# Performance work log

Measured on AMD Instinct MI355X. Metric: run time of the kernel, lower is better.

## Reference

```python
import jax, jax.numpy as jnp
import numpy as np

EPS = 1e-8


def setup_inputs() -> dict:
    key = jax.random.key(0)
    k1, k2, k3 = jax.random.split(key, 3)
    Nq, Nr = 16384, 16384
    return {
        "query_points": jax.random.normal(k1, (Nq, 3), dtype=jnp.float32),
        "ref_points": jax.random.normal(k2, (Nr, 3), dtype=jnp.float32),
        "ref_flow": jax.random.normal(k3, (Nr, 3), dtype=jnp.float32),
        "k": 3,
    }


def reference(query_points, ref_points, ref_flow, k):
    # torch.cdist: Euclidean distance matrix [Nq, Nr]
    q2 = jnp.sum(query_points * query_points, axis=-1, keepdims=True)   # [Nq,1]
    r2 = jnp.sum(ref_points * ref_points, axis=-1)                      # [Nr]
    d2 = q2 + r2[None, :] - 2.0 * (query_points @ ref_points.T)        # [Nq,Nr]
    dist = jnp.sqrt(jnp.maximum(d2, 0.0))
    # topk smallest distances
    neg_top, knn_idx = jax.lax.top_k(-dist, k)                          # [Nq,k]
    knn_dist = -neg_top
    # inverse-distance weights, normalized
    weights = 1.0 / (knn_dist + EPS)
    weights = weights / jnp.sum(weights, axis=1, keepdims=True)
    # gather neighbor flows and reduce: [Nq,k,3] -> [Nq,3]
    knn_flow = ref_flow[knn_idx]
    return jnp.sum(weights[..., None] * knn_flow, axis=1)
```

## Files before the change

kernel.cpp:

```cpp
#include <hip/hip_runtime.h>
#include <math.h>

#define G      32
#define NCELLS (G * G * G)
#define LOF    (-6.0f)
#define HH     0.375f
#define INVH   (1.0f / 0.375f)
#define DELTA  1e-3f
#define NCHUNK 16
#define R2ACC  (HH * HH)
#define SCB    128
#define SCC    (NCELLS / SCB)

__device__ __forceinline__ int cell_coord(float x) {
    int c = (int)floorf((x - LOF) * INVH);
    c = c < 0 ? 0 : c;
    return c > G - 1 ? G - 1 : c;
}
__device__ __forceinline__ int imax2(int a, int b) { return a > b ? a : b; }
__device__ __forceinline__ int imin2(int a, int b) { return a < b ? a : b; }
__device__ __forceinline__ float rdfl(float v) {
    return __int_as_float(__builtin_amdgcn_readfirstlane(__float_as_int(v)));
}

#define LEXINSERT(dv, jv) do {                                        \
    float d_ = (dv); int j_ = (jv);                                   \
    bool l0 = (d_ < e0) || ((d_ == e0) && (j_ < i0));                 \
    bool l1 = (d_ < e1) || ((d_ == e1) && (j_ < i1));                 \
    bool l2 = (d_ < e2) || ((d_ == e2) && (j_ < i2));                 \
    int   ni0 = l0 ? j_ : i0;                                         \
    int   ni1 = l0 ? i0 : (l1 ? j_ : i1);                             \
    int   ni2 = l1 ? i1 : (l2 ? j_ : i2);                             \
    float ne0 = l0 ? d_ : e0;                                         \
    float ne1 = l0 ? e0 : (l1 ? d_ : e1);                             \
    float ne2 = l1 ? e1 : (l2 ? d_ : e2);                             \
    e0 = ne0; e1 = ne1; e2 = ne2; i0 = ni0; i1 = ni1; i2 = ni2;       \
} while (0)

#define SCAN_RUN(lo_, hi_) do {                                       \
    for (int u = (lo_) + lane; u < (hi_); u += 64) {                  \
        float4 rr = srt[u];                                           \
        float xx = rr.x * rr.x;                                       \
        float yy = rr.y * rr.y;                                       \
        float zz = rr.z * rr.z;                                       \
        float r2 = (xx + yy) + zz;                                    \
        float td = qx * rr.x;                                         \
        td = fmaf(qy, rr.y, td);                                      \
        td = fmaf(qz, rr.z, td);                                      \
        float aa = q2 + r2;                                           \
        float dd = fmaf(-2.0f, td, aa);                               \
        int jj = __float_as_int(rr.w);                                \
        LEXINSERT(dd, jj);                                            \
    }                                                                 \
} while (0)

#define MERGE64() do {                                                \
    _Pragma("unroll")                                                 \
    for (int mk_ = 1; mk_ < 64; mk_ <<= 1) {                          \
        float f0 = __shfl_xor(e0, mk_, 64);                           \
        float f1 = __shfl_xor(e1, mk_, 64);                           \
        float f2 = __shfl_xor(e2, mk_, 64);                           \
        int   g0 = __shfl_xor(i0, mk_, 64);                           \
        int   g1 = __shfl_xor(i1, mk_, 64);                           \
        int   g2 = __shfl_xor(i2, mk_, 64);                           \
        LEXINSERT(f0, g0);                                            \
        LEXINSERT(f1, g1);                                            \
        LEXINSERT(f2, g2);                                            \
    }                                                                 \
} while (0)

#define MERGE32() do {                                                \
    _Pragma("unroll")                                                 \
    for (int mk_ = 1; mk_ < 32; mk_ <<= 1) {                          \
        float f0 = __shfl_xor(e0, mk_, 64);                           \
        float f1 = __shfl_xor(e1, mk_, 64);                           \
        float f2 = __shfl_xor(e2, mk_, 64);                           \
        int   g0 = __shfl_xor(i0, mk_, 64);                           \
        int   g1 = __shfl_xor(i1, mk_, 64);                           \
        int   g2 = __shfl_xor(i2, mk_, 64);                           \
        LEXINSERT(f0, g0);                                            \
        LEXINSERT(f1, g1);                                            \
        LEXINSERT(f2, g2);                                            \
    }                                                                 \
} while (0)

#define EPILOGUE() do {                                               \
    e0 = fmaxf(e0, 0.0f);                                             \
    e1 = fmaxf(e1, 0.0f);                                             \
    e2 = fmaxf(e2, 0.0f);                                             \
    float s0 = sqrtf(e0);                                             \
    float s1 = sqrtf(e1);                                             \
    float s2 = sqrtf(e2);                                             \
    float w0 = 1.0f / (s0 + 1e-8f);                                   \
    float w1 = 1.0f / (s1 + 1e-8f);                                   \
    float w2 = 1.0f / (s2 + 1e-8f);                                   \
    float wsum = (w0 + w1) + w2;                                      \
    w0 = w0 / wsum; w1 = w1 / wsum; w2 = w2 / wsum;                   \
    float f0x = flow[i0*3+0], f0y = flow[i0*3+1], f0z = flow[i0*3+2]; \
    float f1x = flow[i1*3+0], f1y = flow[i1*3+1], f1z = flow[i1*3+2]; \
    float f2x = flow[i2*3+0], f2y = flow[i2*3+1], f2z = flow[i2*3+2]; \
    out[q*3+0] = (w0 * f0x + w1 * f1x) + w2 * f2x;                    \
    out[q*3+1] = (w0 * f0y + w1 * f1y) + w2 * f2y;                    \
    out[q*3+2] = (w0 * f0z + w1 * f1z) + w2 * f2z;                    \
} while (0)

__global__ __launch_bounds__(256) void zero_ints(int* __restrict__ p, int n) {
    int i = blockIdx.x * 256 + threadIdx.x;
    if (i < n) p[i] = 0;
}

__global__ __launch_bounds__(256) void bin_count(
    const float* __restrict__ ref, int* __restrict__ cnt, int Nr) {
    int j = blockIdx.x * 256 + threadIdx.x;
    if (j >= Nr) return;
    int cx = cell_coord(ref[3 * j + 0]);
    int cy = cell_coord(ref[3 * j + 1]);
    int cz = cell_coord(ref[3 * j + 2]);
    atomicAdd(&cnt[(cz * G + cy) * G + cx], 1);
}

__global__ __launch_bounds__(256) void scan1(
    const int* __restrict__ cnt, int* __restrict__ off, int* __restrict__ bsum) {
    __shared__ int wt[4];
    int tid = threadIdx.x, b = blockIdx.x;
    int base = b * SCC;
    int lane = tid & 63, wid = tid >> 6;
    int v = cnt[base + tid];
    int incl = v;
#pragma unroll
    for (int sh = 1; sh < 64; sh <<= 1) {
        int t = __shfl_up(incl, sh, 64);
        if (lane >= sh) incl += t;
    }
    if (lane == 63) wt[wid] = incl;
    __syncthreads();
    if (tid == 0) {
        int run = 0;
#pragma unroll
        for (int w = 0; w < 4; ++w) { int t = wt[w]; wt[w] = run; run += t; }
    }
    __syncthreads();
    int excl = wt[wid] + incl - v;
    off[base + tid] = excl;
    if (tid == SCC - 1) bsum[b] = excl + v;
}

__global__ __launch_bounds__(256) void scan2(
    const int* __restrict__ bsum, int* __restrict__ off, int* __restrict__ cur) {
    __shared__ int red[4];
    __shared__ int bo;
    int tid = threadIdx.x, b = blockIdx.x;
    int lane = tid & 63, wid = tid >> 6;
    int m = (tid < b) ? bsum[tid] : 0;
#pragma unroll
    for (int mk = 1; mk < 64; mk <<= 1) m += __shfl_xor(m, mk, 64);
    if (lane == 0) red[wid] = m;
    __syncthreads();
    if (tid == 0) bo = red[0] + red[1] + red[2] + red[3];
    __syncthreads();
    int boff = bo;
    int base = b * SCC;
    int t = off[base + tid] + boff;
    off[base + tid] = t;
    cur[base + tid] = t;
    if (b == SCB - 1 && tid == SCC - 1) off[NCELLS] = boff + bsum[b];
}

__global__ __launch_bounds__(256) void bin_fill(
    const float* __restrict__ ref, int* __restrict__ cur,
    float4* __restrict__ srt, int Nr) {
    int j = blockIdx.x * 256 + threadIdx.x;
    if (j >= Nr) return;
    float x = ref[3 * j + 0], y = ref[3 * j + 1], z = ref[3 * j + 2];
    int cx = cell_coord(x), cy = cell_coord(y), cz = cell_coord(z);
    int cell = (cz * G + cy) * G + cx;
    int pos = atomicAdd(&cur[cell], 1);
    srt[pos] = make_float4(x, y, z, __int_as_float(j));
}

#define MAPIDX(u_, out_) do {                                         \
    int t_ = (u_) + b0;                                               \
    t_ = ((u_) >= p1) ? ((u_) + b1) : t_;                             \
    t_ = ((u_) >= p2) ? ((u_) + b2) : t_;                             \
    t_ = ((u_) >= p3) ? ((u_) + b3) : t_;                             \
    t_ = ((u_) >= p4) ? ((u_) + b4) : t_;                             \
    t_ = ((u_) >= p5) ? ((u_) + b5) : t_;                             \
    t_ = ((u_) >= p6) ? ((u_) + b6) : t_;                             \
    t_ = ((u_) >= p7) ? ((u_) + b7) : t_;                             \
    t_ = ((u_) >= p8) ? ((u_) + b8) : t_;                             \
    (out_) = t_;                                                      \
} while (0)

#define BODY(rr_) do {                                                \
    float xx = (rr_).x * (rr_).x;                                     \
    float yy = (rr_).y * (rr_).y;                                     \
    float zz = (rr_).z * (rr_).z;                                     \
    float r2v = (xx + yy) + zz;                                       \
    float td = qx * (rr_).x;                                          \
    td = fmaf(qy, (rr_).y, td);                                       \
    td = fmaf(qz, (rr_).z, td);                                       \
    float aa = q2 + r2v;                                              \
    float dd = fmaf(-2.0f, td, aa);                                   \
    int jj = __float_as_int((rr_).w);                                 \
    LEXINSERT(dd, jj);                                                \
} while (0)

__global__ __launch_bounds__(256) void knn27(
    const float* __restrict__ qpts, const float4* __restrict__ srt,
    const int* __restrict__ off, const float* __restrict__ flow,
    float* __restrict__ out, int* __restrict__ qlist,
    int* __restrict__ nflag, int Nq) {
#pragma clang fp contract(off)
    int sl = threadIdx.x & 31;
    int q  = blockIdx.x * 8 + (threadIdx.x >> 5);
    bool qv = q < Nq;
    int qc = qv ? q : 0;

    float qx = qpts[3 * qc + 0];
    float qy = qpts[3 * qc + 1];
    float qz = qpts[3 * qc + 2];
    float q2 = (qx * qx + qy * qy) + qz * qz;

    int cx = cell_coord(qx), cy = cell_coord(qy), cz = cell_coord(qz);

    int dz = sl / 3 - 1, dy = sl % 3 - 1;
    int zr = cz + dz, yr = cy + dy;
    bool vrow = (sl < 9) && qv && (zr >= 0) && (zr < G) && (yr >= 0) && (yr < G);
    int xlo = imax2(cx - 1, 0), xhi = imin2(cx + 1, G - 1);
    int vlo = 0, vhi = 0;
    if (vrow) {
        int rowbase = (zr * G + yr) * G;
        vlo = off[rowbase + xlo];
        vhi = off[rowbase + xhi + 1];
    }
    int cnt = vhi - vlo;

    int incl = cnt;
#pragma unroll
    for (int sh = 1; sh <= 8; sh <<= 1) {
        int t = __shfl_up(incl, sh, 32);
        if (sl >= sh) incl += t;
    }
    int total = __shfl(incl, 8, 32);
    int prex  = incl - cnt;

    int p1 = __shfl(prex, 1, 32), p2 = __shfl(prex, 2, 32);
    int p3 = __shfl(prex, 3, 32), p4 = __shfl(prex, 4, 32);
    int p5 = __shfl(prex, 5, 32), p6 = __shfl(prex, 6, 32);
    int p7 = __shfl(prex, 7, 32), p8 = __shfl(prex, 8, 32);
    int b0 = __shfl(vlo, 0, 32);
    int b1 = __shfl(vlo, 1, 32) - p1;
    int b2 = __shfl(vlo, 2, 32) - p2;
    int b3 = __shfl(vlo, 3, 32) - p3;
    int b4 = __shfl(vlo, 4, 32) - p4;
    int b5 = __shfl(vlo, 5, 32) - p5;
    int b6 = __shfl(vlo, 6, 32) - p6;
    int b7 = __shfl(vlo, 7, 32) - p7;
    int b8 = __shfl(vlo, 8, 32) - p8;

    const float FINF = __builtin_inff();
    float e0 = FINF, e1 = FINF, e2 = FINF;
    int   i0 = 0x7fffffff, i1 = 0x7fffffff, i2 = 0x7fffffff;

    int u = sl;
    if (u < total) {
        int idx;
        MAPIDX(u, idx);
        float4 rr = srt[idx];
        for (u += 32; u < total; u += 32) {
            int idx2;
            MAPIDX(u, idx2);
            float4 rn = srt[idx2];
            BODY(rr);
            rr = rn;
        }
        BODY(rr);
    }

    MERGE32();

    bool ok = (e2 + DELTA < R2ACC);
    if (sl == 0 && qv) {
        if (ok) {
            EPILOGUE();
        } else {
            int pos = atomicAdd(nflag, 1);
            qlist[pos] = q;
        }
    }
}

__global__ __launch_bounds__(256) void brute_chunk(
    const float* __restrict__ qpts, const float4* __restrict__ srt,
    const int* __restrict__ qlist, const int* __restrict__ nflag,
    float2* __restrict__ cand, int Nr) {
#pragma clang fp contract(off)
    int lane = threadIdx.x & 63;
    int wav  = (blockIdx.x * 256 + threadIdx.x) >> 6;
    int nWaves = (gridDim.x * 256) >> 6;
    int nItems = nflag[0] * NCHUNK;
    int CS = (Nr + NCHUNK - 1) / NCHUNK;

    for (int item = wav; item < nItems; item += nWaves) {
        int f = item / NCHUNK;
        int chunk = item - f * NCHUNK;
        int q = qlist[f];
        float qx = rdfl(qpts[3 * q + 0]);
        float qy = rdfl(qpts[3 * q + 1]);
        float qz = rdfl(qpts[3 * q + 2]);
        float q2 = (qx * qx + qy * qy) + qz * qz;

        int lo = chunk * CS;
        int hi = imin2(lo + CS, Nr);

        const float FINF = __builtin_inff();
        float e0 = FINF, e1 = FINF, e2 = FINF;
        int   i0 = 0x7fffffff, i1 = 0x7fffffff, i2 = 0x7fffffff;

        SCAN_RUN(lo, hi);
        MERGE64();

        if (lane == 0) {
            cand[item * 3 + 0] = make_float2(e0, __int_as_float(i0));
            cand[item * 3 + 1] = make_float2(e1, __int_as_float(i1));
            cand[item * 3 + 2] = make_float2(e2, __int_as_float(i2));
        }
    }
}

__global__ __launch_bounds__(256) void brute_merge(
    const int* __restrict__ qlist, const int* __restrict__ nflag,
    const float2* __restrict__ cand, const float* __restrict__ flow,
    float* __restrict__ out) {
#pragma clang fp contract(off)
    int lane = threadIdx.x & 63;
    int wav  = (blockIdx.x * 256 + threadIdx.x) >> 6;
    int nWaves = (gridDim.x * 256) >> 6;
    int n = nflag[0];

    for (int f = wav; f < n; f += nWaves) {
        int q = qlist[f];
        const float FINF = __builtin_inff();
        float e0 = FINF, e1 = FINF, e2 = FINF;
        int   i0 = 0x7fffffff, i1 = 0x7fffffff, i2 = 0x7fffffff;
        if (lane < 3 * NCHUNK) {
            float2 cc = cand[f * (3 * NCHUNK) + lane];
            e0 = cc.x;
            i0 = __float_as_int(cc.y);
        }
        MERGE64();
        if (lane == 0) EPILOGUE();
    }
}

extern "C" void kernel_launch(void* const* d_in, const int* in_sizes, int n_in,
                              void* d_out, int out_size, void* d_ws, size_t ws_size,
                              hipStream_t stream) {
    const float* qp   = (const float*)d_in[0];
    const float* ref  = (const float*)d_in[1];
    const float* flow = (const float*)d_in[2];
    float* out = (float*)d_out;

    int Nq = in_sizes[0] / 3;
    int Nr = in_sizes[1] / 3;

    char* ws = (char*)d_ws;
    float4* srt = (float4*)ws;
    size_t o = (size_t)Nr * sizeof(float4);
    int* off    = (int*)(ws + o);  o += (size_t)(NCELLS + 1) * sizeof(int);
    int* cur    = (int*)(ws + o);  o += (size_t)NCELLS * sizeof(int);
    int* cnt    = (int*)(ws + o);  o += (size_t)(NCELLS + 1) * sizeof(int);
    int* nflag  = cnt + NCELLS;
    int* qlist  = (int*)(ws + o);  o += (size_t)Nq * sizeof(int);
    int* bsum   = (int*)(ws + o);  o += (size_t)SCB * sizeof(int);
    o = (o + 15) & ~(size_t)15;
    float2* cand = (float2*)(ws + o);
    o += (size_t)Nq * 3 * NCHUNK * sizeof(float2);

    zero_ints<<<(NCELLS + 1 + 255) / 256, 256, 0, stream>>>(cnt, NCELLS + 1);
    bin_count<<<(Nr + 255) / 256, 256, 0, stream>>>(ref, cnt, Nr);
    scan1<<<SCB, 256, 0, stream>>>(cnt, off, bsum);
    scan2<<<SCB, 256, 0, stream>>>(bsum, off, cur);
    bin_fill<<<(Nr + 255) / 256, 256, 0, stream>>>(ref, cur, srt, Nr);

    int nBlocks = (Nq + 7) / 8;
    knn27<<<nBlocks, 256, 0, stream>>>(qp, srt, off, flow, out, qlist, nflag, Nq);
    brute_chunk<<<1024, 256, 0, stream>>>(qp, srt, qlist, nflag, cand, Nr);
    brute_merge<<<256, 256, 0, stream>>>(qlist, nflag, cand, flow, out);
}
```

Before: 78.75 us.

## Bin query points into spatial cells so neighbouring queries share blocks

Query points are now counted, scanned and scattered into the same cell-sorted buffer as the reference points, using a second bank of grid cells. The knn kernel then walks queries in cell order, so the warps of a block search nearby cells and reuse cached reference data. The cost is extra counting and scatter work over the queries and a scan twice as large. Results are still written to each query's original index.

```diff
diff --git a/kernel.cpp b/kernel.cpp
--- a/kernel.cpp
+++ b/kernel.cpp
@@ -3,14 +3,15 @@
 
 #define G      32
 #define NCELLS (G * G * G)
+#define TOTC   (2 * NCELLS)
 #define LOF    (-6.0f)
 #define HH     0.375f
 #define INVH   (1.0f / 0.375f)
 #define DELTA  1e-3f
 #define NCHUNK 16
 #define R2ACC  (HH * HH)
-#define SCB    128
-#define SCC    (NCELLS / SCB)
+#define SCB    256
+#define SCC    (TOTC / SCB)
 
 __device__ __forceinline__ int cell_coord(float x) {
     int c = (int)floorf((x - LOF) * INVH);
@@ -109,14 +110,22 @@
     if (i < n) p[i] = 0;
 }
 
-__global__ __launch_bounds__(256) void bin_count(
-    const float* __restrict__ ref, int* __restrict__ cnt, int Nr) {
+__global__ __launch_bounds__(256) void bin_count2(
+    const float* __restrict__ ref, const float* __restrict__ qpts,
+    int* __restrict__ cnt, int Nr, int Nq) {
     int j = blockIdx.x * 256 + threadIdx.x;
-    if (j >= Nr) return;
-    int cx = cell_coord(ref[3 * j + 0]);
-    int cy = cell_coord(ref[3 * j + 1]);
-    int cz = cell_coord(ref[3 * j + 2]);
-    atomicAdd(&cnt[(cz * G + cy) * G + cx], 1);
+    if (j < Nr) {
+        int cx = cell_coord(ref[3 * j + 0]);
+        int cy = cell_coord(ref[3 * j + 1]);
+        int cz = cell_coord(ref[3 * j + 2]);
+        atomicAdd(&cnt[(cz * G + cy) * G + cx], 1);
+    } else if (j < Nr + Nq) {
+        int k = j - Nr;
+        int cx = cell_coord(qpts[3 * k + 0]);
+        int cy = cell_coord(qpts[3 * k + 1]);
+        int cz = cell_coord(qpts[3 * k + 2]);
+        atomicAdd(&cnt[NCELLS + (cz * G + cy) * G + cx], 1);
+    }
 }
 
 __global__ __launch_bounds__(256) void scan1(
@@ -163,19 +172,25 @@
     int t = off[base + tid] + boff;
     off[base + tid] = t;
     cur[base + tid] = t;
-    if (b == SCB - 1 && tid == SCC - 1) off[NCELLS] = boff + bsum[b];
-}
-
-__global__ __launch_bounds__(256) void bin_fill(
-    const float* __restrict__ ref, int* __restrict__ cur,
-    float4* __restrict__ srt, int Nr) {
+    if (b == SCB - 1 && tid == SCC - 1) off[TOTC] = boff + bsum[b];
+}
+
+__global__ __launch_bounds__(256) void bin_fill2(
+    const float* __restrict__ ref, const float* __restrict__ qpts,
+    int* __restrict__ cur, float4* __restrict__ big, int Nr, int Nq) {
     int j = blockIdx.x * 256 + threadIdx.x;
-    if (j >= Nr) return;
-    float x = ref[3 * j + 0], y = ref[3 * j + 1], z = ref[3 * j + 2];
-    int cx = cell_coord(x), cy = cell_coord(y), cz = cell_coord(z);
-    int cell = (cz * G + cy) * G + cx;
-    int pos = atomicAdd(&cur[cell], 1);
-    srt[pos] = make_float4(x, y, z, __int_as_float(j));
+    if (j < Nr) {
+        float x = ref[3 * j + 0], y = ref[3 * j + 1], z = ref[3 * j + 2];
+        int cell = (cell_coord(z) * G + cell_coord(y)) * G + cell_coord(x);
+        int pos = atomicAdd(&cur[cell], 1);
+        big[pos] = make_float4(x, y, z, __int_as_float(j));
+    } else if (j < Nr + Nq) {
+        int k = j - Nr;
+        float x = qpts[3 * k + 0], y = qpts[3 * k + 1], z = qpts[3 * k + 2];
+        int cell = NCELLS + (cell_coord(z) * G + cell_coord(y)) * G + cell_coord(x);
+        int pos = atomicAdd(&cur[cell], 1);
+        big[pos] = make_float4(x, y, z, __int_as_float(k));
+    }
 }
 
 #define MAPIDX(u_, out_) do {                                         \
@@ -206,19 +221,19 @@
 } while (0)
 
 __global__ __launch_bounds__(256) void knn27(
-    const float* __restrict__ qpts, const float4* __restrict__ srt,
-    const int* __restrict__ off, const float* __restrict__ flow,
-    float* __restrict__ out, int* __restrict__ qlist,
-    int* __restrict__ nflag, int Nq) {
+    const float4* __restrict__ big, const int* __restrict__ off,
+    const float* __restrict__ flow, float* __restrict__ out,
+    int* __restrict__ qlist, int* __restrict__ nflag, int Nr, int Nq) {
 #pragma clang fp contract(off)
+    const float4* __restrict__ srt = big;
     int sl = threadIdx.x & 31;
-    int q  = blockIdx.x * 8 + (threadIdx.x >> 5);
-    bool qv = q < Nq;
-    int qc = qv ? q : 0;
-
-    float qx = qpts[3 * qc + 0];
-    float qy = qpts[3 * qc + 1];
-    float qz = qpts[3 * qc + 2];
+    int sq = blockIdx.x * 8 + (threadIdx.x >> 5);
+    bool qv = sq < Nq;
+    int sqc = qv ? sq : 0;
+
+    float4 qq = big[(size_t)Nr + sqc];
+    float qx = qq.x, qy = qq.y, qz = qq.z;
+    int   q  = __float_as_int(qq.w);
     float q2 = (qx * qx + qy * qy) + qz * qz;
 
     int cx = cell_coord(qx), cy = cell_coord(qy), cz = cell_coord(qz);
@@ -365,26 +380,26 @@
     int Nr = in_sizes[1] / 3;
 
     char* ws = (char*)d_ws;
-    float4* srt = (float4*)ws;
-    size_t o = (size_t)Nr * sizeof(float4);
-    int* off    = (int*)(ws + o);  o += (size_t)(NCELLS + 1) * sizeof(int);
-    int* cur    = (int*)(ws + o);  o += (size_t)NCELLS * sizeof(int);
-    int* cnt    = (int*)(ws + o);  o += (size_t)(NCELLS + 1) * sizeof(int);
-    int* nflag  = cnt + NCELLS;
+    float4* big = (float4*)ws;
+    size_t o = (size_t)(Nr + Nq) * sizeof(float4);
+    int* off    = (int*)(ws + o);  o += (size_t)(TOTC + 1) * sizeof(int);
+    int* cur    = (int*)(ws + o);  o += (size_t)TOTC * sizeof(int);
+    int* cnt    = (int*)(ws + o);  o += (size_t)(TOTC + 1) * sizeof(int);
+    int* nflag  = cnt + TOTC;
     int* qlist  = (int*)(ws + o);  o += (size_t)Nq * sizeof(int);
     int* bsum   = (int*)(ws + o);  o += (size_t)SCB * sizeof(int);
     o = (o + 15) & ~(size_t)15;
     float2* cand = (float2*)(ws + o);
     o += (size_t)Nq * 3 * NCHUNK * sizeof(float2);
 
-    zero_ints<<<(NCELLS + 1 + 255) / 256, 256, 0, stream>>>(cnt, NCELLS + 1);
-    bin_count<<<(Nr + 255) / 256, 256, 0, stream>>>(ref, cnt, Nr);
+    zero_ints<<<(TOTC + 1 + 255) / 256, 256, 0, stream>>>(cnt, TOTC + 1);
+    bin_count2<<<(Nr + Nq + 255) / 256, 256, 0, stream>>>(ref, qp, cnt, Nr, Nq);
     scan1<<<SCB, 256, 0, stream>>>(cnt, off, bsum);
     scan2<<<SCB, 256, 0, stream>>>(bsum, off, cur);
-    bin_fill<<<(Nr + 255) / 256, 256, 0, stream>>>(ref, cur, srt, Nr);
+    bin_fill2<<<(Nr + Nq + 255) / 256, 256, 0, stream>>>(ref, qp, cur, big, Nr, Nq);
 
     int nBlocks = (Nq + 7) / 8;
-    knn27<<<nBlocks, 256, 0, stream>>>(qp, srt, off, flow, out, qlist, nflag, Nq);
-    brute_chunk<<<1024, 256, 0, stream>>>(qp, srt, qlist, nflag, cand, Nr);
+    knn27<<<nBlocks, 256, 0, stream>>>(big, off, flow, out, qlist, nflag, Nr, Nq);
+    brute_chunk<<<1024, 256, 0, stream>>>(qp, big, qlist, nflag, cand, Nr);
     brute_merge<<<256, 256, 0, stream>>>(qlist, nflag, cand, flow, out);
 }
```

New measurement: 73.69 us. 6.4% less time.
